# Kernel tuning notes

Hardware: AMD Instinct MI355X
Metric: run time of the kernel (lower is better)

## Reference

```python
import jax, jax.numpy as jnp
import numpy as np

B, C, H, W = 4, 256, 64, 64
NB = 4            # num_bands
CR = C // 4       # channel-attention reduction


def _conv(x, w, b, pad):
    y = jax.lax.conv_general_dilated(x, w, window_strides=(1, 1),
                                     padding=[(pad, pad), (pad, pad)],
                                     dimension_numbers=('NCHW', 'OIHW', 'NCHW'))
    return y + b[None, :, None, None]


def setup_inputs() -> dict:
    key = jax.random.key(0)
    ks = jax.random.split(key, 16)
    d = {}
    d['x'] = jax.random.normal(ks[0], (B, C, H, W), dtype=jnp.float32)
    # spline weights / scalers: one (out,in) matrix per band
    d['spline_w'] = jax.random.normal(ks[1], (NB, C, C), dtype=jnp.float32) / np.sqrt(C)
    d['scalers'] = jax.random.uniform(ks[2], (NB, C, C), minval=0.9, maxval=1.1, dtype=jnp.float32)
    # feature_transform: conv3x3 -> BN -> ReLU -> conv3x3
    d['ft_w1'] = jax.random.normal(ks[3], (C, C, 3, 3), dtype=jnp.float32) / np.sqrt(C * 9)
    d['ft_b1'] = jnp.zeros((C,), jnp.float32)
    d['bn_g'] = jnp.ones((C,), jnp.float32)
    d['bn_b'] = jnp.zeros((C,), jnp.float32)
    d['bn_m'] = 0.01 * jax.random.normal(ks[4], (C,), dtype=jnp.float32)
    d['bn_v'] = jnp.ones((C,), jnp.float32)
    d['ft_w2'] = jax.random.normal(ks[5], (C, C, 3, 3), dtype=jnp.float32) / np.sqrt(C * 9)
    d['ft_b2'] = jnp.zeros((C,), jnp.float32)
    # channel attention: 1x1 convs C -> C/4 -> C
    d['ca_w1'] = jax.random.normal(ks[6], (CR, C, 1, 1), dtype=jnp.float32) / np.sqrt(C)
    d['ca_b1'] = jnp.zeros((CR,), jnp.float32)
    d['ca_w2'] = jax.random.normal(ks[7], (C, CR, 1, 1), dtype=jnp.float32) / np.sqrt(CR)
    d['ca_b2'] = jnp.zeros((C,), jnp.float32)
    # spatial attention: conv3x3 2 -> 1
    d['sa_w'] = jax.random.normal(ks[8], (1, 2, 3, 3), dtype=jnp.float32) / np.sqrt(18)
    d['sa_b'] = jnp.zeros((1,), jnp.float32)
    return d


def _forward(x, spline_w, scalers, ft_w1, ft_b1, bn_g, bn_b, bn_m, bn_v,
             ft_w2, ft_b2, ca_w1, ca_b1, ca_w2, ca_b2, sa_w, sa_b):
    eps = 1e-5

    def feature_transform(t):
        t = _conv(t, ft_w1, ft_b1, 1)
        t = bn_g[None, :, None, None] * (t - bn_m[None, :, None, None]) * \
            jax.lax.rsqrt(bn_v + eps)[None, :, None, None] + bn_b[None, :, None, None]
        t = jax.nn.relu(t)
        return _conv(t, ft_w2, ft_b2, 1)

    # ---- spectral decompose: rfft over channel dim, per-band irfft ----
    xf = x.transpose(0, 2, 3, 1).reshape(-1, C)      # (B*H*W, C)
    F = jnp.fft.rfft(xf, axis=-1)                    # (B*H*W, C//2+1)
    nfreq = F.shape[-1]
    bs = nfreq // NB
    bands = []
    for i in range(NB):
        s = i * bs
        e = nfreq if i == NB - 1 else (i + 1) * bs
        # irfft zero-pads the sliced spectrum back to length C (matches torch)
        bands.append(jnp.fft.irfft(F[:, s:e], n=C, axis=-1).reshape(B, H, W, C))
    xd = jnp.stack(bands, axis=1)                    # (B, NB, H, W, C)

    # NOTE: the original .view(B*NB, C, H, W) on a (B,NB,H,W,C)-contiguous tensor
    # is a raw memory reinterpretation (not a permute); jnp.reshape matches it.
    xd = xd.reshape(B * NB, C, H, W)
    xd = feature_transform(xd)
    xd = xd.reshape(B, NB, H, W, C)

    # ---- attention block (shares feature_transform weights) ----
    t = xd.reshape(B * NB, C, H, W)
    t = feature_transform(t)
    gap = jnp.mean(t, axis=(2, 3), keepdims=True)    # (B*NB, C, 1, 1)
    cw = jax.nn.sigmoid(_conv(jax.nn.gelu(_conv(gap, ca_w1, ca_b1, 0), approximate=False),
                              ca_w2, ca_b2, 0))
    t = t * cw
    avg_out = jnp.mean(t, axis=1, keepdims=True)
    max_out = jnp.max(t, axis=1, keepdims=True)
    sw = jax.nn.sigmoid(_conv(jnp.concatenate([avg_out, max_out], axis=1), sa_w, sa_b, 1))
    t = t * sw
    xd = t.reshape(B, NB, H, W, C)

    # ---- spline stage ----
    # In the source, the Cox-de Boor basis recursion is computed but UNUSED:
    # einsum('bci,oi->bci', band_x, weight) == band_x * weight.sum(0), so the
    # effective math is a per-band, per-feature scaling (dead basis code omitted).
    w_eff = (spline_w * scalers).sum(axis=1)          # (NB, C)
    xv = xd.reshape(B, NB, H * W, C)
    band_out = xv * w_eff[None, :, None, :]
    fused = band_out.mean(axis=1)                     # (B, H*W, C)
    return fused.reshape(B, H, W, C).transpose(0, 3, 1, 2)


def reference(x, spline_w, scalers, ft_w1, ft_b1, bn_g, bn_b, bn_m, bn_v,
              ft_w2, ft_b2, ca_w1, ca_b1, ca_w2, ca_b2, sa_w, sa_b):
    return _forward(x, spline_w, scalers, ft_w1, ft_b1, bn_g, bn_b, bn_m, bn_v,
                    ft_w2, ft_b2, ca_w1, ca_b1, ca_w2, ca_b2, sa_w, sa_b)
```

## Files before the change

### kernel.cpp

```cpp
#include <hip/hip_runtime.h>
#include <hip/hip_bf16.h>


#define CHW   1048576
#define HW    4096

typedef _Float16 f16;
typedef _Float16 f16x8 __attribute__((ext_vector_type(8)));
typedef float    f32x4 __attribute__((ext_vector_type(4)));

__global__ __launch_bounds__(256) void k2_kernel(float* __restrict__ K2) {
    __shared__ float ctab[256];
    const int c = blockIdx.x;
    const int t = threadIdx.x;
    ctab[t] = cosf((float)t * 0.024543692606170259f);
    __syncthreads();
#pragma unroll
    for (int q = 0; q < 4; q++) {
        const int o = q * 256 + t;
        const int s = q * 32;
        const int L = (q == 3) ? 33 : 32;
        float sum = ctab[(s * c) & 255];
        for (int k = 1; k < L; k++) {
            int m = ((s + k) * c + k * (256 - t)) & 255;
            sum += 2.f * ctab[m];
        }
        K2[c * 1024 + o] = sum * 0.00390625f;
    }
}

__global__ __launch_bounds__(256) void wsplit_kernel(const float* __restrict__ w,
                                                     f16* __restrict__ Wh,
                                                     f16* __restrict__ Wl) {
    const int b = blockIdx.x;
    const int tap = b >> 8, oc = b & 255;
    const int ic = threadIdx.x;
    const float v = w[(oc * 256 + ic) * 9 + tap];
    const f16 hi = (f16)v;
    Wh[b * 256 + ic] = hi;
    Wl[b * 256 + ic] = (f16)(v - (float)hi);
}

__global__ __launch_bounds__(256) void small_pre_kernel(
    const float* __restrict__ spw, const float* __restrict__ scl,
    const float* __restrict__ bn_g, const float* __restrict__ bn_b,
    const float* __restrict__ bn_m, const float* __restrict__ bn_v,
    const float* __restrict__ ft_b1, float* __restrict__ weff,
    float* __restrict__ bnscale, float* __restrict__ bnbias) {
    const int c = threadIdx.x;
    const float s = bn_g[c] * rsqrtf(bn_v[c] + 1e-5f);
    bnscale[c] = s;
    bnbias[c] = (ft_b1[c] - bn_m[c]) * s + bn_b[c];
    for (int n = 0; n < 4; n++) {
        float acc = 0.f;
        for (int j = 0; j < 256; j++)
            acc += spw[n * 65536 + j * 256 + c] * scl[n * 65536 + j * 256 + c];
        weff[n * 256 + c] = acc;
    }
}

__global__ __launch_bounds__(256) void decompose_kernel(const float* __restrict__ x,
                                                        const float* __restrict__ K2,
                                                        float* __restrict__ xd) {
    const int o0 = blockIdx.x * 128;
    const int p0 = blockIdx.y * 64;
    const int b = p0 >> 12;
    const int prow = p0 & 4095;
    const int t = threadIdx.x;
    const int pg = t >> 4, og = t & 15;
    __shared__ float As[16][64];
    __shared__ float Bs[16][128];
    float acc[4][8];
#pragma unroll
    for (int i = 0; i < 4; i++)
#pragma unroll
        for (int j = 0; j < 8; j++) acc[i][j] = 0.f;

    for (int c0 = 0; c0 < 256; c0 += 16) {
#pragma unroll
        for (int i = 0; i < 4; i++) {
            int c = (t >> 6) + i * 4;
            As[c][t & 63] = x[b * CHW + (c0 + c) * HW + prow + (t & 63)];
        }
#pragma unroll
        for (int i = 0; i < 8; i++) {
            int l = i * 256 + t;
            Bs[l >> 7][l & 127] = K2[(c0 + (l >> 7)) * 1024 + o0 + (l & 127)];
        }
        __syncthreads();
#pragma unroll
        for (int k = 0; k < 16; k++) {
            float a[4], bb[8];
            *(float4*)a = *(const float4*)&As[k][pg * 4];
            *(float4*)&bb[0] = *(const float4*)&Bs[k][og * 8];
            *(float4*)&bb[4] = *(const float4*)&Bs[k][og * 8 + 4];
#pragma unroll
            for (int i = 0; i < 4; i++)
#pragma unroll
                for (int j = 0; j < 8; j++) acc[i][j] = fmaf(a[i], bb[j], acc[i][j]);
        }
        __syncthreads();
    }
#pragma unroll
    for (int i = 0; i < 4; i++) {
        const int p = prow + pg * 4 + i;
#pragma unroll
        for (int j = 0; j < 8; j++) {
            const int o = o0 + og * 8 + j;
            const int n = o >> 8, cc = o & 255;
            xd[b * 4194304 + n * CHW + p * 256 + cc] = acc[i][j];
        }
    }
}

__global__ __launch_bounds__(256) void xpose_kernel(const float* __restrict__ in,
                                                    f16* __restrict__ Xh,
                                                    f16* __restrict__ Xl) {
    const int bn = blockIdx.y;
    const int tid = blockIdx.x;
    const int k = tid & 15;
    const int cc0 = ((tid >> 4) & 1) * 128;
    const int c0p = (tid >> 5) * 64;
    __shared__ float T[64 * 132];
    const int base = bn * 1048576;
    for (int c = threadIdx.x; c < 2048; c += 256) {
        int cl = c >> 5;
        int ccq = c & 31;
        int pd = (c0p + cl) * 16 + k;
        *(float4*)&T[cl * 132 + ccq * 4] =
            *(const float4*)&in[base + pd * 256 + cc0 + ccq * 4];
    }
    __syncthreads();
    for (int m = threadIdx.x; m < 1024; m += 256) {
        int pl = m >> 3;
        int cq = m & 7;
        f16x8 hi, lo;
#pragma unroll
        for (int j = 0; j < 8; ++j) {
            float v = T[(cq * 8 + j) * 132 + pl];
            f16 h = (f16)v;
            hi[j] = h;
            lo[j] = (f16)(v - (float)h);
        }
        int pp = k * 256 + cc0 + pl;
        int o = base + pp * 256 + c0p + cq * 8;
        *(f16x8*)&Xh[o] = hi;
        *(f16x8*)&Xl[o] = lo;
    }
}

template <int MODE, int PACKED>
__global__ __launch_bounds__(256, 2) void conv_mfma_kernel(
    const f16* __restrict__ Xh, const f16* __restrict__ Xl,
    const f16* __restrict__ Wg_h, const f16* __restrict__ Wg_l,
    const float* __restrict__ scale, const float* __restrict__ bias,
    f16* __restrict__ Oh, f16* __restrict__ Ol, float* __restrict__ Of) {
    const int oc0 = blockIdx.x * 128;
    const int h0 = (blockIdx.y >> 2) * 8;
    const int w0 = (blockIdx.y & 3) * 16;
    const int bn = blockIdx.z;

    __shared__ __align__(16) f16 smem[12800 + 2 * 8192];
    f16* At = smem;
    f16* Ws = smem + 12800;

    const int t = threadIdx.x;
    const int wid = t >> 6, lane = t & 63;
    const int wm = wid >> 1, wn = wid & 1;
    const int lrow = lane & 15, g = lane >> 4;

    const int row_s = t >> 3;
    const int sub_s = t & 7;
    const int half_s = sub_s >> 2, icq_s = sub_s & 3;
    const int swz_s = (sub_s ^ (row_s & 7)) << 3;

    f32x4 acc[4][4];
    const f32x4 z4 = {0.f, 0.f, 0.f, 0.f};
#pragma unroll
    for (int i = 0; i < 4; i++)
#pragma unroll
        for (int j = 0; j < 4; j++) acc[i][j] = z4;

    const int xbase = bn * CHW;

    f16x8 wreg[4];
    {
        const f16* wsrc = (half_s ? Wg_l : Wg_h) + oc0 * 256 + row_s * 256 + icq_s * 8;
#pragma unroll
        for (int k = 0; k < 4; k++) wreg[k] = *(const f16x8*)(wsrc + k * 8192);
    }

#pragma unroll 1
    for (int chunk = 0; chunk < 8; ++chunk) {
        const int ic0 = chunk * 32;
        __syncthreads();
        {
            const f16* xs = (half_s ? Xl : Xh) + xbase + ic0 + icq_s * 8;
#pragma unroll
            for (int i = 0; i < 7; ++i) {
                int c = t + i * 256;
                if (c < 1600) {
                    int pos = row_s + i * 32;
                    int r = pos / 20, col = pos - r * 20;
                    int gy = h0 - 1 + r, gx = w0 - 1 + col;
                    f16x8 v = {};
                    if (col < 18 && (unsigned)gy < 64u && (unsigned)gx < 64u)
                        v = *(const f16x8*)(xs + (gy * 64 + gx) * 256);
                    *(f16x8*)&At[pos * 64 + swz_s] = v;
                }
            }
        }
#pragma unroll
        for (int tap = 0; tap < 9; ++tap) {
            const int ky = tap / 3, kx = tap % 3;
            f16* slab = Ws + (tap & 1) * 8192;
            {
                f16* wdst = &slab[row_s * 64 + swz_s];
#pragma unroll
                for (int k = 0; k < 4; k++) *(f16x8*)(wdst + k * 2048) = wreg[k];
            }
            int ntap = tap + 1, nchunk = chunk;
            if (ntap == 9) { ntap = 0; nchunk = chunk + 1; }
            if (nchunk < 8) {
                const f16* wsrc = (half_s ? Wg_l : Wg_h) + ntap * 65536 +
                                  oc0 * 256 + nchunk * 32 + row_s * 256 + icq_s * 8;
#pragma unroll
                for (int k = 0; k < 4; k++) wreg[k] = *(const f16x8*)(wsrc + k * 8192);
            }
            __syncthreads();
            f16x8 a_h[4], a_l[4], b_h[4], b_l[4];
#pragma unroll
            for (int mf = 0; mf < 4; ++mf) {
                int pos = (wm * 4 + mf + ky) * 20 + (lrow + kx);
                int p7 = (pos & 7) << 3;
                a_h[mf] = *(const f16x8*)&At[pos * 64 + ((g << 3) ^ p7)];
                a_l[mf] = *(const f16x8*)&At[pos * 64 + (((4 + g) << 3) ^ p7)];
            }
#pragma unroll
            for (int nf = 0; nf < 4; ++nf) {
                int ocl = wn * 64 + nf * 16 + lrow;
                int o7 = (ocl & 7) << 3;
                b_h[nf] = *(const f16x8*)&slab[ocl * 64 + ((g << 3) ^ o7)];
                b_l[nf] = *(const f16x8*)&slab[ocl * 64 + (((4 + g) << 3) ^ o7)];
            }
#pragma unroll
            for (int mf = 0; mf < 4; ++mf)
#pragma unroll
                for (int nf = 0; nf < 4; ++nf) {
                    acc[mf][nf] = __builtin_amdgcn_mfma_f32_16x16x32_f16(
                        a_h[mf], b_h[nf], acc[mf][nf], 0, 0, 0);
                    acc[mf][nf] = __builtin_amdgcn_mfma_f32_16x16x32_f16(
                        a_h[mf], b_l[nf], acc[mf][nf], 0, 0, 0);
                    acc[mf][nf] = __builtin_amdgcn_mfma_f32_16x16x32_f16(
                        a_l[mf], b_h[nf], acc[mf][nf], 0, 0, 0);
                }
        }
    }

    if (PACKED == 0) {
#pragma unroll
        for (int nf = 0; nf < 4; ++nf) {
            const int oc = oc0 + wn * 64 + nf * 16 + lrow;
            const float sc = (MODE == 1) ? scale[oc] : 1.f;
            const float bi = bias[oc];
#pragma unroll
            for (int mf = 0; mf < 4; ++mf) {
                const int oh = wm * 4 + mf;
                float4 o;
                float* op = &o.x;
#pragma unroll
                for (int j = 0; j < 4; ++j) {
                    float v = acc[mf][nf][j];
                    op[j] = (MODE == 1) ? fmaxf(v * sc + bi, 0.f) : (v + bi);
                }
                *(float4*)&Of[bn * CHW + oc * HW + (h0 + oh) * 64 + w0 + g * 4] = o;
            }
        }
    } else {
        f16* Th = smem;
        f16* Tl = smem + 8192;
        for (int half = 0; half < 2; ++half) {
            __syncthreads();
            if (wn == half) {
#pragma unroll
                for (int nf = 0; nf < 4; ++nf) {
                    const int oclb = nf * 16 + lrow;
                    const int oc = oc0 + half * 64 + oclb;
                    const float sc = (MODE == 1) ? scale[oc] : 1.f;
                    const float bi = bias[oc];
#pragma unroll
                    for (int mf = 0; mf < 4; ++mf) {
                        const int pb = (wm * 4 + mf) * 16;
#pragma unroll
                        for (int j = 0; j < 4; ++j) {
                            float v = acc[mf][nf][j];
                            v = (MODE == 1) ? fmaxf(v * sc + bi, 0.f) : (v + bi);
                            f16 hi = (f16)v;
                            int p = pb + g * 4 + j;
                            int idx = p * 64 + (oclb ^ ((p & 7) << 3));
                            Th[idx] = hi;
                            Tl[idx] = (f16)(v - (float)hi);
                        }
                    }
                }
            }
            __syncthreads();
            for (int c = t; c < 1024; c += 256) {
                int p = c >> 3, q = c & 7;
                int src = p * 64 + ((q ^ (p & 7)) << 3);
                int gp = xbase + ((h0 + (p >> 4)) * 64 + w0 + (p & 15)) * 256 +
                         oc0 + half * 64 + q * 8;
                *(f16x8*)&Oh[gp] = *(const f16x8*)&Th[src];
                *(f16x8*)&Ol[gp] = *(const f16x8*)&Tl[src];
            }
        }
    }
}

__global__ __launch_bounds__(256) void gap_kernel(const float* __restrict__ t2,
                                                  float* __restrict__ gap) {
    const int bc = blockIdx.x;
    const float* p = t2 + bc * HW;
    float s = 0.f;
    for (int i = threadIdx.x; i < 4096; i += 256) s += p[i];
    __shared__ float red[256];
    red[threadIdx.x] = s;
    __syncthreads();
    for (int off = 128; off > 0; off >>= 1) {
        if (threadIdx.x < off) red[threadIdx.x] += red[threadIdx.x + off];
        __syncthreads();
    }
    if (threadIdx.x == 0) gap[bc] = red[0] * (1.f / 4096.f);
}

__global__ __launch_bounds__(256) void ca_kernel(
    const float* __restrict__ gap, const float* __restrict__ w1,
    const float* __restrict__ b1, const float* __restrict__ w2,
    const float* __restrict__ b2, float* __restrict__ cw) {
    const int bn = blockIdx.x;
    const int t = threadIdx.x;
    __shared__ float gsh[256];
    __shared__ float hid[64];
    gsh[t] = gap[bn * 256 + t];
    __syncthreads();
    if (t < 64) {
        float a = b1[t];
        for (int c = 0; c < 256; c++) a += w1[t * 256 + c] * gsh[c];
        hid[t] = 0.5f * a * (1.f + erff(a * 0.70710678118654752f));
    }
    __syncthreads();
    float a = b2[t];
    for (int j = 0; j < 64; j++) a += w2[t * 64 + j] * hid[j];
    cw[bn * 256 + t] = 1.f / (1.f + expf(-a));
}

__global__ __launch_bounds__(256) void samap_kernel(const float* __restrict__ t2,
                                                    const float* __restrict__ cw,
                                                    float* __restrict__ avg,
                                                    float* __restrict__ mx) {
    const int bn = blockIdx.x >> 4;
    const int h = (blockIdx.x & 15) * 4 + (threadIdx.x >> 6);
    const int w = threadIdx.x & 63;
    const float* p = t2 + bn * CHW + h * 64 + w;
    float s = 0.f, m = -3.4e38f;
    for (int c = 0; c < 256; c++) {
        float v = p[c * HW] * cw[bn * 256 + c];
        s += v;
        m = fmaxf(m, v);
    }
    avg[bn * HW + h * 64 + w] = s * (1.f / 256.f);
    mx[bn * HW + h * 64 + w] = m;
}

__global__ __launch_bounds__(256) void sw_kernel(const float* __restrict__ avg,
                                                 const float* __restrict__ mx,
                                                 const float* __restrict__ saw,
                                                 const float* __restrict__ sab,
                                                 float* __restrict__ sw) {
    const int bn = blockIdx.x >> 4;
    const int h = (blockIdx.x & 15) * 4 + (threadIdx.x >> 6);
    const int w = threadIdx.x & 63;
    float a = sab[0];
#pragma unroll
    for (int ky = 0; ky < 3; ky++) {
        int y = h + ky - 1;
        if ((unsigned)y >= 64u) continue;
#pragma unroll
        for (int kx = 0; kx < 3; kx++) {
            int x = w + kx - 1;
            if ((unsigned)x >= 64u) continue;
            int idx = bn * HW + y * 64 + x;
            a += saw[ky * 3 + kx] * avg[idx] + saw[9 + ky * 3 + kx] * mx[idx];
        }
    }
    sw[bn * HW + h * 64 + w] = 1.f / (1.f + expf(-a));
}

__global__ __launch_bounds__(256) void fuse_kernel(const float* __restrict__ t2,
                                                   const float* __restrict__ cw,
                                                   const float* __restrict__ sw,
                                                   const float* __restrict__ weff,
                                                   float* __restrict__ out) {
    const int b = blockIdx.x >> 6;
    const int ho = blockIdx.x & 63;
    const int co = threadIdx.x;
    __shared__ float T[256 * 33];
    float we[4];
#pragma unroll
    for (int n = 0; n < 4; n++) we[n] = weff[n * 256 + co];

    for (int hf = 0; hf < 2; hf++) {
        for (int wo = 0; wo < 32; wo++) {
            const int o = ho * 16384 + (hf * 32 + wo) * 256 + co;
            const int ct = o >> 12;
            const int ht = (o >> 6) & 63;
            const int wt = o & 63;
            float acc = 0.f;
#pragma unroll
            for (int n = 0; n < 4; n++) {
                const int bn = b * 4 + n;
                acc += we[n] * t2[bn * CHW + o] * cw[bn * 256 + ct] *
                       sw[bn * HW + ht * 64 + wt];
            }
            T[co * 33 + wo] = 0.25f * acc;
        }
        __syncthreads();
        for (int it = 0; it < 32; it++) {
            const int l = it * 256 + threadIdx.x;
            const int c2 = l >> 5, w2 = l & 31;
            out[b * CHW + c2 * HW + ho * 64 + hf * 32 + w2] = T[c2 * 33 + w2];
        }
        __syncthreads();
    }
}

extern "C" void kernel_launch(void* const* d_in, const int* in_sizes, int n_in,
                              void* d_out, int out_size, void* d_ws, size_t ws_size,
                              hipStream_t stream) {
    const float* x        = (const float*)d_in[0];
    const float* spline_w = (const float*)d_in[1];
    const float* scalers  = (const float*)d_in[2];
    const float* ft_w1    = (const float*)d_in[3];
    const float* ft_b1    = (const float*)d_in[4];
    const float* bn_g     = (const float*)d_in[5];
    const float* bn_b     = (const float*)d_in[6];
    const float* bn_m     = (const float*)d_in[7];
    const float* bn_v     = (const float*)d_in[8];
    const float* ft_w2    = (const float*)d_in[9];
    const float* ft_b2    = (const float*)d_in[10];
    const float* ca_w1    = (const float*)d_in[11];
    const float* ca_b1    = (const float*)d_in[12];
    const float* ca_w2    = (const float*)d_in[13];
    const float* ca_b2    = (const float*)d_in[14];
    const float* sa_w     = (const float*)d_in[15];
    const float* sa_b     = (const float*)d_in[16];

    char* p = (char*)d_ws;
    auto alloc = [&](size_t bytes) {
        char* r = p;
        p += (bytes + 255) & ~(size_t)255;
        return r;
    };
    float* K2      = (float*)alloc(262144 * 4);
    f16*   W1h     = (f16*)alloc(589824 * 2);
    f16*   W1l     = (f16*)alloc(589824 * 2);
    f16*   W2h     = (f16*)alloc(589824 * 2);
    f16*   W2l     = (f16*)alloc(589824 * 2);
    float* weff    = (float*)alloc(1024 * 4);
    float* bnscale = (float*)alloc(256 * 4);
    float* bnbias  = (float*)alloc(256 * 4);
    float* gapb    = (float*)alloc(4096 * 4);
    float* cwb     = (float*)alloc(4096 * 4);
    float* avgm    = (float*)alloc(65536 * 4);
    float* mxm     = (float*)alloc(65536 * 4);
    float* swm     = (float*)alloc(65536 * 4);
    const size_t HALF = (size_t)16777216 * 2;
    char* R1 = alloc(2 * HALF);
    char* R2 = alloc(2 * HALF);
    float* bufA = (float*)R1;
    f16*   Y1h  = (f16*)R1;
    f16*   Y1l  = (f16*)(R1 + HALF);
    f16*   X1h  = (f16*)R2;
    f16*   X1l  = (f16*)(R2 + HALF);
    f16*   Y2h  = (f16*)R2;
    f16*   Y2l  = (f16*)(R2 + HALF);
    float* t2   = (float*)R2;

    k2_kernel<<<256, 256, 0, stream>>>(K2);
    wsplit_kernel<<<2304, 256, 0, stream>>>(ft_w1, W1h, W1l);
    wsplit_kernel<<<2304, 256, 0, stream>>>(ft_w2, W2h, W2l);
    small_pre_kernel<<<1, 256, 0, stream>>>(spline_w, scalers, bn_g, bn_b, bn_m,
                                            bn_v, ft_b1, weff, bnscale, bnbias);
    decompose_kernel<<<dim3(8, 256), 256, 0, stream>>>(x, K2, bufA);
    xpose_kernel<<<dim3(128, 16), 256, 0, stream>>>(bufA, X1h, X1l);

    dim3 cgrid(2, 32, 16);
    conv_mfma_kernel<1, 1><<<cgrid, 256, 0, stream>>>(X1h, X1l, W1h, W1l,
                                                      bnscale, bnbias, Y1h, Y1l, nullptr);
    conv_mfma_kernel<0, 1><<<cgrid, 256, 0, stream>>>(Y1h, Y1l, W2h, W2l,
                                                      nullptr, ft_b2, Y2h, Y2l, nullptr);
    conv_mfma_kernel<1, 1><<<cgrid, 256, 0, stream>>>(Y2h, Y2l, W1h, W1l,
                                                      bnscale, bnbias, Y1h, Y1l, nullptr);
    conv_mfma_kernel<0, 0><<<cgrid, 256, 0, stream>>>(Y1h, Y1l, W2h, W2l,
                                                      nullptr, ft_b2, nullptr, nullptr, t2);

    gap_kernel<<<4096, 256, 0, stream>>>(t2, gapb);
    ca_kernel<<<16, 256, 0, stream>>>(gapb, ca_w1, ca_b1, ca_w2, ca_b2, cwb);
    samap_kernel<<<256, 256, 0, stream>>>(t2, cwb, avgm, mxm);
    sw_kernel<<<256, 256, 0, stream>>>(avgm, mxm, sa_w, sa_b, swm);
    fuse_kernel<<<256, 256, 0, stream>>>(t2, cwb, swm, weff, (float*)d_out);
}
```

Before: 1.090 ms.

## Load conv weights directly from global into MFMA registers, drop LDS weight staging

```diff
diff --git a/kernel.cpp b/kernel.cpp
--- a/kernel.cpp
+++ b/kernel.cpp
@@ -160,9 +160,8 @@
     const int w0 = (blockIdx.y & 3) * 16;
     const int bn = blockIdx.z;
 
-    __shared__ __align__(16) f16 smem[12800 + 2 * 8192];
+    __shared__ __align__(16) f16 smem[16384];
     f16* At = smem;
-    f16* Ws = smem + 12800;
 
     const int t = threadIdx.x;
     const int wid = t >> 6, lane = t & 63;
@@ -183,17 +182,21 @@
 
     const int xbase = bn * CHW;
 
-    f16x8 wreg[4];
-    {
-        const f16* wsrc = (half_s ? Wg_l : Wg_h) + oc0 * 256 + row_s * 256 + icq_s * 8;
-#pragma unroll
-        for (int k = 0; k < 4; k++) wreg[k] = *(const f16x8*)(wsrc + k * 8192);
-    }
+    const size_t wlane = (size_t)(oc0 + wn * 64 + lrow) * 256 + g * 8;
+    const f16* wh_base = Wg_h + wlane;
+    const f16* wl_base = Wg_l + wlane;
+
+    f16x8 bh[2][4], bl[2][4];
 
 #pragma unroll 1
     for (int chunk = 0; chunk < 8; ++chunk) {
         const int ic0 = chunk * 32;
         __syncthreads();
+#pragma unroll
+        for (int nf = 0; nf < 4; ++nf) {
+            bh[0][nf] = *(const f16x8*)(wh_base + nf * 4096 + ic0);
+            bl[0][nf] = *(const f16x8*)(wl_base + nf * 4096 + ic0);
+        }
         {
             const f16* xs = (half_s ? Xl : Xh) + xbase + ic0 + icq_s * 8;
 #pragma unroll
@@ -210,25 +213,20 @@
                 }
             }
         }
+        __syncthreads();
 #pragma unroll
         for (int tap = 0; tap < 9; ++tap) {
             const int ky = tap / 3, kx = tap % 3;
-            f16* slab = Ws + (tap & 1) * 8192;
-            {
-                f16* wdst = &slab[row_s * 64 + swz_s];
-#pragma unroll
-                for (int k = 0; k < 4; k++) *(f16x8*)(wdst + k * 2048) = wreg[k];
-            }
-            int ntap = tap + 1, nchunk = chunk;
-            if (ntap == 9) { ntap = 0; nchunk = chunk + 1; }
-            if (nchunk < 8) {
-                const f16* wsrc = (half_s ? Wg_l : Wg_h) + ntap * 65536 +
-                                  oc0 * 256 + nchunk * 32 + row_s * 256 + icq_s * 8;
-#pragma unroll
-                for (int k = 0; k < 4; k++) wreg[k] = *(const f16x8*)(wsrc + k * 8192);
-            }
-            __syncthreads();
-            f16x8 a_h[4], a_l[4], b_h[4], b_l[4];
+            const int pc = tap & 1;
+            if (tap < 8) {
+                const size_t wo = (size_t)(tap + 1) * 65536 + ic0;
+#pragma unroll
+                for (int nf = 0; nf < 4; ++nf) {
+                    bh[pc ^ 1][nf] = *(const f16x8*)(wh_base + wo + nf * 4096);
+                    bl[pc ^ 1][nf] = *(const f16x8*)(wl_base + wo + nf * 4096);
+                }
+            }
+            f16x8 a_h[4], a_l[4];
 #pragma unroll
             for (int mf = 0; mf < 4; ++mf) {
                 int pos = (wm * 4 + mf + ky) * 20 + (lrow + kx);
@@ -237,22 +235,15 @@
                 a_l[mf] = *(const f16x8*)&At[pos * 64 + (((4 + g) << 3) ^ p7)];
             }
 #pragma unroll
-            for (int nf = 0; nf < 4; ++nf) {
-                int ocl = wn * 64 + nf * 16 + lrow;
-                int o7 = (ocl & 7) << 3;
-                b_h[nf] = *(const f16x8*)&slab[ocl * 64 + ((g << 3) ^ o7)];
-                b_l[nf] = *(const f16x8*)&slab[ocl * 64 + (((4 + g) << 3) ^ o7)];
-            }
-#pragma unroll
             for (int mf = 0; mf < 4; ++mf)
 #pragma unroll
                 for (int nf = 0; nf < 4; ++nf) {
                     acc[mf][nf] = __builtin_amdgcn_mfma_f32_16x16x32_f16(
-                        a_h[mf], b_h[nf], acc[mf][nf], 0, 0, 0);
+                        a_h[mf], bh[pc][nf], acc[mf][nf], 0, 0, 0);
                     acc[mf][nf] = __builtin_amdgcn_mfma_f32_16x16x32_f16(
-                        a_h[mf], b_l[nf], acc[mf][nf], 0, 0, 0);
+                        a_h[mf], bl[pc][nf], acc[mf][nf], 0, 0, 0);
                     acc[mf][nf] = __builtin_amdgcn_mfma_f32_16x16x32_f16(
-                        a_l[mf], b_h[nf], acc[mf][nf], 0, 0, 0);
+                        a_l[mf], bh[pc][nf], acc[mf][nf], 0, 0, 0);
                 }
         }
     }
```

Result: slower. 1.517 ms (+39.1%).
